# Kernel optimization log

Measured on AMD Instinct MI355X. Metric: run time of the kernel, lower is better.

## Reference

```python
import jax, jax.numpy as jnp
import numpy as np

B, H, V, L = 4096, 1024, 64, 16  # batch, hidden_size, msg_vocsize, max_msg_len


def setup_inputs() -> dict:
    key = jax.random.key(0)
    ks = jax.random.split(key, 10)
    s = 1.0 / np.sqrt(H)
    return {
        "encoder_hidden": jax.random.normal(ks[0], (B, H), jnp.float32),
        "encoder_cell": jax.random.normal(ks[1], (B, H), jnp.float32),
        "W_ih": jax.random.uniform(ks[2], (4 * H, H), jnp.float32, -s, s),
        "W_hh": jax.random.uniform(ks[3], (4 * H, H), jnp.float32, -s, s),
        "b_ih": jax.random.uniform(ks[4], (4 * H,), jnp.float32, -s, s),
        "b_hh": jax.random.uniform(ks[5], (4 * H,), jnp.float32, -s, s),
        "W_out": jax.random.uniform(ks[6], (V, H), jnp.float32, -s, s),
        "b_out": jax.random.uniform(ks[7], (V,), jnp.float32, -s, s),
        "init_input": jnp.zeros((1, H), jnp.float32),  # nn.Parameter initialized to zeros
        "msg_embedding": jax.random.normal(ks[8], (V, H), jnp.float32),
    }


def reference(encoder_hidden, encoder_cell, W_ih, W_hh, b_ih, b_hh,
              W_out, b_out, init_input, msg_embedding):
    batch = encoder_hidden.shape[0]
    x0 = jnp.broadcast_to(init_input, (batch, H))

    def step(carry, _):
        h, c, x, logp = carry
        x = jax.nn.relu(x)
        gates = x @ W_ih.T + b_ih + h @ W_hh.T + b_hh  # [B, 4H]
        i, f, g, o = jnp.split(gates, 4, axis=-1)      # torch LSTMCell gate order
        i, f, o = jax.nn.sigmoid(i), jax.nn.sigmoid(f), jax.nn.sigmoid(o)
        g = jnp.tanh(g)
        c = f * c + i * g
        h = o * jnp.tanh(c)
        logits = h @ W_out.T + b_out                   # [B, V]
        probs = jax.nn.softmax(logits, axis=1)
        pred = jax.nn.one_hot(jnp.argmax(probs, axis=1), V, dtype=probs.dtype)
        logp = logp + jnp.log(jnp.sum(probs * pred, axis=1))
        x = pred @ msg_embedding                       # [B, H]
        return (h, c, x, logp), (pred, logits)

    init = (encoder_hidden, encoder_cell, x0, jnp.zeros((batch,), encoder_hidden.dtype))
    (_, _, _, log_probs), (message, digits) = jax.lax.scan(step, init, None, length=L)
    mask = jnp.ones((L, 1, batch), encoder_hidden.dtype)
    return message, mask, digits, log_probs
```

## Files before the change

kernel.cpp:

```cpp
#include <hip/hip_runtime.h>
#include <math.h>

#define HD    1024
#define BATCH 4096
#define VOC   64
#define MSGL  16
#define KH    1024
#define NG    4096

typedef _Float16 f16;
typedef _Float16 f16x8 __attribute__((ext_vector_type(8)));
typedef _Float16 f16x4 __attribute__((ext_vector_type(4)));
typedef float    f32x4 __attribute__((ext_vector_type(4)));

__device__ __forceinline__ void splt(float v, f16& hi, f16& lo) {
    f16 h = (f16)v;
    hi = h;
    lo = (f16)(v - (float)h);
}

__device__ __forceinline__ float sigm_f(float x) {
    return __builtin_amdgcn_rcpf(1.0f + __builtin_amdgcn_exp2f(-1.44269504088896f * x));
}
__device__ __forceinline__ float tanh_f(float x) {
    return 1.0f - 2.0f * __builtin_amdgcn_rcpf(1.0f + __builtin_amdgcn_exp2f(2.88539008177793f * x));
}

__device__ __forceinline__ int orig_n(int np) {
    const int bxx = np >> 8, rem = np & 255;
    const int jh = rem >> 6, g = (rem >> 4) & 3, cnn = rem & 15;
    return g * 1024 + bxx * 64 + jh * 16 + cnn;
}
__device__ __forceinline__ int j_of(int np) {
    const int bxx = np >> 8, rem = np & 255;
    const int jh = rem >> 6, cnn = rem & 15;
    return bxx * 64 + jh * 16 + cnn;
}

__device__ __forceinline__ void async16(void* lds, const void* g) {
    __builtin_amdgcn_global_load_lds(
        (const __attribute__((address_space(1))) void*)g,
        (__attribute__((address_space(3))) void*)lds, 16, 0, 0);
}

__device__ __forceinline__ int swz(int row, int gran) {
    return row * 128 + ((gran ^ (row & 7)) << 4);
}

__device__ __forceinline__ void stage(char* ldsbase, const f16* hi, const f16* lo,
                                      int gbase, int k0, int r, int tid) {
    const int o   = (r * 512 + tid) * 16;
    const int row = o >> 7;
    const int gp  = (o >> 4) & 7;
    const int g   = gp ^ (row & 7);
    const f16* src = (g < 4 ? hi : lo) + (size_t)(gbase + row) * KH + k0 + (g & 3) * 8;
    async16(ldsbase + o, src);
}

__global__ __launch_bounds__(512, 2) void gemm_fused(
    const f16* __restrict__ Hh, const f16* __restrict__ Hl,
    const f16* __restrict__ Whi, const f16* __restrict__ Wlo,
    const float* __restrict__ XG, const int* __restrict__ ambuf,
    float* __restrict__ cbuf,
    f16* __restrict__ HhN, f16* __restrict__ HlN, int t)
{
    __shared__ char smem[132096];
    __shared__ int sAm[256];

    const int tid  = threadIdx.x;
    const int lane = tid & 63;
    const int wv   = tid >> 6;
    const int wm   = wv >> 2;
    const int wn   = wv & 3;
    const int bm   = blockIdx.y * 256;
    const int bnp  = blockIdx.x * 256;
    const int rl   = lane & 15;
    const int kg   = lane >> 4;

    f32x4 acc[8][4];
#pragma unroll
    for (int i = 0; i < 8; ++i)
#pragma unroll
        for (int g = 0; g < 4; ++g) acc[i][g] = f32x4{0.f, 0.f, 0.f, 0.f};

    if (tid < 256) sAm[tid] = (t == 0) ? 64 : ambuf[bm + tid];

#pragma unroll
    for (int r = 0; r < 4; ++r) stage(smem,         Hh,  Hl,  bm,  0, r, tid);
#pragma unroll
    for (int r = 0; r < 4; ++r) stage(smem + 32768, Whi, Wlo, bnp, 0, r, tid);

    for (int kt = 0; kt < 32; ++kt) {
        const char* cb = smem + (kt & 1) * 65536;
        char* nb = smem + ((kt + 1) & 1) * 65536;
        const int kn = ((kt + 1) & 31) * 32;

        asm volatile("s_waitcnt vmcnt(4)" ::: "memory");
        asm volatile("s_barrier" ::: "memory");

#pragma unroll
        for (int r = 0; r < 4; ++r) stage(nb, Hh, Hl, bm, kn, r, tid);

        asm volatile("s_waitcnt vmcnt(4)" ::: "memory");
        asm volatile("s_barrier" ::: "memory");

        f16x8 bh[4], bl[4];
#pragma unroll
        for (int f = 0; f < 4; ++f) {
            const int row = wn * 64 + f * 16 + rl;
            bh[f] = *(const f16x8*)(cb + 32768 + swz(row, kg));
            bl[f] = *(const f16x8*)(cb + 32768 + swz(row, kg + 4));
        }
#pragma unroll
        for (int r = 0; r < 4; ++r) stage(nb + 32768, Whi, Wlo, bnp, kn, r, tid);

        __builtin_amdgcn_s_setprio(1);
#pragma unroll
        for (int f = 0; f < 8; ++f) {
            const int row = wm * 128 + f * 16 + rl;
            const f16x8 ah = *(const f16x8*)(cb + swz(row, kg));
            const f16x8 al = *(const f16x8*)(cb + swz(row, kg + 4));
#pragma unroll
            for (int g = 0; g < 4; ++g) {
                acc[f][g] = __builtin_amdgcn_mfma_f32_16x16x32_f16(ah, bh[g], acc[f][g], 0, 0, 0);
                acc[f][g] = __builtin_amdgcn_mfma_f32_16x16x32_f16(ah, bl[g], acc[f][g], 0, 0, 0);
                acc[f][g] = __builtin_amdgcn_mfma_f32_16x16x32_f16(al, bh[g], acc[f][g], 0, 0, 0);
            }
        }
        __builtin_amdgcn_s_setprio(0);
    }

    asm volatile("s_waitcnt vmcnt(0)" ::: "memory");
    __syncthreads();

    float* sXG = (float*)smem;
    f16*   hHi = (f16*)(smem + 66560);
    f16*   hLo = (f16*)(smem + 99328);
    const int jb = blockIdx.x * 64;

#pragma unroll
    for (int i = 0; i < 9; ++i) {
        const int idx = i * 512 + tid;
        if (idx < 65 * 64) {
            const int v  = idx >> 6;
            const int c4 = (idx & 63) * 4;
            *(float4*)&sXG[v * 256 + c4] =
                *(const float4*)&XG[(size_t)v * NG + bnp + c4];
        }
    }
    __syncthreads();

    const int q    = lane >> 4;
    const int lcol = wn * 16 + rl;
    const int jglob = jb + lcol;
#pragma unroll
    for (int i = 0; i < 8; ++i) {
#pragma unroll
        for (int rg = 0; rg < 4; ++rg) {
            const int lrow = wm * 128 + i * 16 + q * 4 + rg;
            const int v = sAm[lrow];
            const float4 xg = *(const float4*)&sXG[v * 256 + lcol * 4];
            const size_t ci = (size_t)(bm + lrow) * HD + jglob;
            const float cold = cbuf[ci];
            const float I = sigm_f(acc[i][0][rg] + xg.x);
            const float F = sigm_f(acc[i][1][rg] + xg.y);
            const float G = tanh_f(acc[i][2][rg] + xg.z);
            const float O = sigm_f(acc[i][3][rg] + xg.w);
            const float cc = F * cold + I * G;
            const float hh = O * tanh_f(cc);
            cbuf[ci] = cc;
            f16 hi_, lo_;
            splt(hh, hi_, lo_);
            hHi[lrow * 64 + lcol] = hi_;
            hLo[lrow * 64 + lcol] = lo_;
        }
    }
    __syncthreads();

#pragma unroll
    for (int r = 0; r < 8; ++r) {
        const int idx = r * 512 + tid;
        const int row = idx >> 4;
        const int c4  = (idx & 15) * 4;
        *(f16x4*)&HhN[(size_t)(bm + row) * HD + jb + c4] = *(f16x4*)&hHi[row * 64 + c4];
        *(f16x4*)&HlN[(size_t)(bm + row) * HD + jb + c4] = *(f16x4*)&hLo[row * 64 + c4];
    }
}

__global__ __launch_bounds__(256) void logits_step(
    const f16* __restrict__ Hh, const f16* __restrict__ Hl,
    const float* __restrict__ W_outT, const float* __restrict__ b_out,
    float* __restrict__ omsg, float* __restrict__ odig,
    float* __restrict__ ologp, int* __restrict__ ambuf, int t)
{
    const int lane = threadIdx.x & 63;
    const int wv   = threadIdx.x >> 6;
    const int r0   = blockIdx.x * 8 + wv * 2;

    float a0 = 0.f, a1 = 0.f;
    const f16* hh0 = Hh + (size_t)r0 * HD;
    const f16* hl0 = Hl + (size_t)r0 * HD;
    const f16* hh1 = hh0 + HD;
    const f16* hl1 = hl0 + HD;
    for (int k = 0; k < HD; k += 4) {
        const float w0 = W_outT[(k + 0) * 64 + lane];
        const float w1 = W_outT[(k + 1) * 64 + lane];
        const float w2 = W_outT[(k + 2) * 64 + lane];
        const float w3 = W_outT[(k + 3) * 64 + lane];
        const f16x4 vh0 = *(const f16x4*)&hh0[k];
        const f16x4 vl0 = *(const f16x4*)&hl0[k];
        const f16x4 vh1 = *(const f16x4*)&hh1[k];
        const f16x4 vl1 = *(const f16x4*)&hl1[k];
        a0 += w0 * ((float)vh0[0] + (float)vl0[0]) + w1 * ((float)vh0[1] + (float)vl0[1])
            + w2 * ((float)vh0[2] + (float)vl0[2]) + w3 * ((float)vh0[3] + (float)vl0[3]);
        a1 += w0 * ((float)vh1[0] + (float)vl1[0]) + w1 * ((float)vh1[1] + (float)vl1[1])
            + w2 * ((float)vh1[2] + (float)vl1[2]) + w3 * ((float)vh1[3] + (float)vl1[3]);
    }
    const float bo = b_out[lane];
    const float accs[2] = {a0, a1};

#pragma unroll
    for (int r = 0; r < 2; ++r) {
        const int row = r0 + r;
        const float lg = accs[r] + bo;

        float m = lg; int am = lane;
#pragma unroll
        for (int d = 1; d < 64; d <<= 1) {
            const float om = __shfl_xor(m, d);
            const int   oa = __shfl_xor(am, d);
            if (om > m || (om == m && oa < am)) { m = om; am = oa; }
        }
        float s = expf(lg - m);
#pragma unroll
        for (int d = 1; d < 64; d <<= 1) s += __shfl_xor(s, d);

        odig[(size_t)row * VOC + lane] = lg;
        omsg[(size_t)row * VOC + lane] = (lane == am) ? 1.0f : 0.0f;
        if (lane == 0) {
            const float prev = (t == 0) ? 0.0f : ologp[row];
            ologp[row] = prev - logf(s);
            ambuf[row] = am;
        }
    }
}

__global__ __launch_bounds__(256) void xg_kernel(
    const float* __restrict__ W_ih, const float* __restrict__ rembT,
    const float* __restrict__ rembX0, const float* __restrict__ bR,
    float* __restrict__ XG)
{
    __shared__ float sW[4][1024];
    const int lane = threadIdx.x & 63;
    const int wv   = threadIdx.x >> 6;
    const int np   = blockIdx.x * 4 + wv;
    const int orig = orig_n(np);
    const float* wr = W_ih + (size_t)orig * HD;
#pragma unroll
    for (int c = 0; c < 4; ++c)
        *(float4*)&sW[wv][c * 256 + lane * 4] = *(const float4*)&wr[c * 256 + lane * 4];
    __syncthreads();

    float acc = 0.f, acc0 = 0.f;
#pragma unroll 4
    for (int k = 0; k < HD; ++k) {
        const float w = sW[wv][k];
        acc  += w * rembT[k * 64 + lane];
        acc0 += w * rembX0[k];
    }
    const float b = bR[np];
    const int g = (np >> 4) & 3;
    const int pos = j_of(np) * 4 + g;
    XG[(size_t)lane * NG + pos] = acc + b;
    if (lane == 0) XG[(size_t)64 * NG + pos] = acc0 + b;
}

__global__ __launch_bounds__(256) void prep_w(
    const float* __restrict__ W_hh, f16* __restrict__ Whi, f16* __restrict__ Wlo)
{
    const long long idx = ((long long)blockIdx.x * 256 + threadIdx.x) * 4;
    const int np = (int)(idx >> 10);
    const int k  = (int)(idx & 1023);
    const float4 v = *(const float4*)&W_hh[(size_t)orig_n(np) * HD + k];
    f16x4 vh, vl; f16 hi_, lo_;
    splt(v.x, hi_, lo_); vh[0] = hi_; vl[0] = lo_;
    splt(v.y, hi_, lo_); vh[1] = hi_; vl[1] = lo_;
    splt(v.z, hi_, lo_); vh[2] = hi_; vl[2] = lo_;
    splt(v.w, hi_, lo_); vh[3] = hi_; vl[3] = lo_;
    *(f16x4*)&Whi[idx] = vh;
    *(f16x4*)&Wlo[idx] = vl;
}

__global__ __launch_bounds__(256) void prep_h(
    const float* __restrict__ ench, f16* __restrict__ Hh, f16* __restrict__ Hl)
{
    const int idx = (blockIdx.x * 256 + threadIdx.x) * 4;
    const float4 v = *(const float4*)&ench[idx];
    f16x4 vh, vl; f16 hi_, lo_;
    splt(v.x, hi_, lo_); vh[0] = hi_; vl[0] = lo_;
    splt(v.y, hi_, lo_); vh[1] = hi_; vl[1] = lo_;
    splt(v.z, hi_, lo_); vh[2] = hi_; vl[2] = lo_;
    splt(v.w, hi_, lo_); vh[3] = hi_; vl[3] = lo_;
    *(f16x4*)&Hh[idx] = vh;
    *(f16x4*)&Hl[idx] = vl;
}

__global__ __launch_bounds__(256) void prep_c(
    const float* __restrict__ encc, float* __restrict__ cbuf)
{
    const int idx = (blockIdx.x * 256 + threadIdx.x) * 4;
    *(float4*)&cbuf[idx] = *(const float4*)&encc[idx];
}

__global__ __launch_bounds__(256) void prep_small(
    const float* __restrict__ W_out, const float* __restrict__ b_ih,
    const float* __restrict__ b_hh, const float* __restrict__ emb,
    const float* __restrict__ x0,
    float* __restrict__ W_outT, float* __restrict__ rembT,
    float* __restrict__ rembX0, float* __restrict__ bR, float* __restrict__ mask)
{
    const int i = blockIdx.x * 256 + threadIdx.x;
    mask[i] = 1.0f;
    const int v = i >> 10, k = i & 1023;
    W_outT[k * 64 + v] = W_out[i];
    rembT[k * 64 + v] = fmaxf(emb[i], 0.f);
    if (i < 1024) rembX0[i] = fmaxf(x0[i], 0.f);
    if (i < NG) {
        const int orig = orig_n(i);
        bR[i] = b_ih[orig] + b_hh[orig];
    }
}

extern "C" void kernel_launch(void* const* d_in, const int* in_sizes, int n_in,
                              void* d_out, int out_size, void* d_ws, size_t ws_size,
                              hipStream_t stream)
{
    const float* ench  = (const float*)d_in[0];
    const float* encc  = (const float*)d_in[1];
    const float* W_ih  = (const float*)d_in[2];
    const float* W_hh  = (const float*)d_in[3];
    const float* b_ih  = (const float*)d_in[4];
    const float* b_hh  = (const float*)d_in[5];
    const float* W_out = (const float*)d_in[6];
    const float* b_out = (const float*)d_in[7];
    const float* x0    = (const float*)d_in[8];
    const float* emb   = (const float*)d_in[9];
    float* out = (float*)d_out;

    char* ws = (char*)d_ws;
    f16*   Hh[2]  = { (f16*)(ws + ((size_t) 0 << 20)), (f16*)(ws + ((size_t)16 << 20)) };
    f16*   Hl[2]  = { (f16*)(ws + ((size_t) 8 << 20)), (f16*)(ws + ((size_t)24 << 20)) };
    f16*   Whr    = (f16*)(ws + ((size_t)32 << 20));
    f16*   Wlr    = (f16*)(ws + ((size_t)40 << 20));
    float* cbuf   = (float*)(ws + ((size_t)48 << 20));
    float* W_outT = (float*)(ws + ((size_t)64 << 20));
    float* rembT  = (float*)(ws + ((size_t)65 << 20));
    float* rembX0 = (float*)(ws + ((size_t)66 << 20));
    float* bR     = (float*)(ws + ((size_t)66 << 20) + 8192);
    float* XG     = (float*)(ws + ((size_t)67 << 20));
    int*   ambuf  = (int*)  (ws + ((size_t)69 << 20));

    float* out_msg0 = out;
    float* out_mask = out + (size_t)MSGL * BATCH * VOC;
    float* out_dig0 = out_mask + (size_t)MSGL * BATCH;
    float* out_logp = out_dig0 + (size_t)MSGL * BATCH * VOC;

    prep_w<<<4096, 256, 0, stream>>>(W_hh, Whr, Wlr);
    prep_h<<<4096, 256, 0, stream>>>(ench, Hh[0], Hl[0]);
    prep_c<<<4096, 256, 0, stream>>>(encc, cbuf);
    prep_small<<<256, 256, 0, stream>>>(W_out, b_ih, b_hh, emb, x0,
                                        W_outT, rembT, rembX0, bR, out_mask);
    xg_kernel<<<1024, 256, 0, stream>>>(W_ih, rembT, rembX0, bR, XG);

    for (int t = 0; t < MSGL; ++t) {
        const int cur = t & 1, nxt = cur ^ 1;
        gemm_fused<<<dim3(16, 16), 512, 0, stream>>>(
            Hh[cur], Hl[cur], Whr, Wlr, XG, ambuf, cbuf, Hh[nxt], Hl[nxt], t);
        logits_step<<<512, 256, 0, stream>>>(
            Hh[nxt], Hl[nxt], W_outT, b_out,
            out_msg0 + (size_t)t * BATCH * VOC,
            out_dig0 + (size_t)t * BATCH * VOC,
            out_logp, ambuf, t);
    }
}
```

Measured before the change: 2.359 ms.

## Switch gemm_fused to 128-row tiles with triple-buffered LDS pipeline

The recurrent GEMM tile is cut from 256x256 to 128x256 and the grid grows from 256 to 512 blocks launched as a 1D grid. The LDS pipeline goes from two buffers to three, prefetching two k-steps ahead with one barrier per iteration instead of two. This should give more blocks to fill the CUs and hide load latency better. In exchange, each block reuses the W tile over fewer rows, and LDS growing to 144KB drops occupancy to one block per CU.

```diff
diff --git a/kernel.cpp b/kernel.cpp
--- a/kernel.cpp
+++ b/kernel.cpp
@@ -48,8 +48,8 @@
 }
 
 __device__ __forceinline__ void stage(char* ldsbase, const f16* hi, const f16* lo,
-                                      int gbase, int k0, int r, int tid) {
-    const int o   = (r * 512 + tid) * 16;
+                                      int gbase, int k0, int idx) {
+    const int o   = idx * 16;
     const int row = o >> 7;
     const int gp  = (o >> 4) & 7;
     const int g   = gp ^ (row & 7);
@@ -57,69 +57,74 @@
     async16(ldsbase + o, src);
 }
 
-__global__ __launch_bounds__(512, 2) void gemm_fused(
+__global__ __launch_bounds__(512, 1) void gemm_fused(
     const f16* __restrict__ Hh, const f16* __restrict__ Hl,
     const f16* __restrict__ Whi, const f16* __restrict__ Wlo,
     const float* __restrict__ XG, const int* __restrict__ ambuf,
     float* __restrict__ cbuf,
     f16* __restrict__ HhN, f16* __restrict__ HlN, int t)
 {
-    __shared__ char smem[132096];
-    __shared__ int sAm[256];
+    __shared__ char smem[147456];
+    __shared__ int sAm[128];
 
     const int tid  = threadIdx.x;
     const int lane = tid & 63;
     const int wv   = tid >> 6;
     const int wm   = wv >> 2;
     const int wn   = wv & 3;
-    const int bm   = blockIdx.y * 256;
-    const int bnp  = blockIdx.x * 256;
+    const int d    = blockIdx.x;
+    const int by   = d >> 4;
+    const int bx   = d & 15;
+    const int bm   = by * 128;
+    const int bnp  = bx * 256;
     const int rl   = lane & 15;
     const int kg   = lane >> 4;
 
-    f32x4 acc[8][4];
-#pragma unroll
-    for (int i = 0; i < 8; ++i)
+    f32x4 acc[4][4];
+#pragma unroll
+    for (int i = 0; i < 4; ++i)
 #pragma unroll
         for (int g = 0; g < 4; ++g) acc[i][g] = f32x4{0.f, 0.f, 0.f, 0.f};
 
-    if (tid < 256) sAm[tid] = (t == 0) ? 64 : ambuf[bm + tid];
-
-#pragma unroll
-    for (int r = 0; r < 4; ++r) stage(smem,         Hh,  Hl,  bm,  0, r, tid);
-#pragma unroll
-    for (int r = 0; r < 4; ++r) stage(smem + 32768, Whi, Wlo, bnp, 0, r, tid);
+    if (tid < 128) sAm[tid] = (t == 0) ? 64 : ambuf[bm + tid];
+
+    char* s0 = smem;
+    char* s1 = smem + 49152;
+    char* s2 = smem + 98304;
+
+#pragma unroll
+    for (int r = 0; r < 2; ++r) stage(s0,         Hh,  Hl,  bm,  0,  r * 512 + tid);
+#pragma unroll
+    for (int r = 0; r < 4; ++r) stage(s0 + 16384, Whi, Wlo, bnp, 0,  r * 512 + tid);
+#pragma unroll
+    for (int r = 0; r < 2; ++r) stage(s1,         Hh,  Hl,  bm,  32, r * 512 + tid);
+#pragma unroll
+    for (int r = 0; r < 4; ++r) stage(s1 + 16384, Whi, Wlo, bnp, 32, r * 512 + tid);
 
     for (int kt = 0; kt < 32; ++kt) {
-        const char* cb = smem + (kt & 1) * 65536;
-        char* nb = smem + ((kt + 1) & 1) * 65536;
-        const int kn = ((kt + 1) & 31) * 32;
-
-        asm volatile("s_waitcnt vmcnt(4)" ::: "memory");
+        const int kn = ((kt + 2) & 31) * 32;
+
+        asm volatile("s_waitcnt vmcnt(6)" ::: "memory");
         asm volatile("s_barrier" ::: "memory");
 
 #pragma unroll
-        for (int r = 0; r < 4; ++r) stage(nb, Hh, Hl, bm, kn, r, tid);
-
-        asm volatile("s_waitcnt vmcnt(4)" ::: "memory");
-        asm volatile("s_barrier" ::: "memory");
+        for (int r = 0; r < 2; ++r) stage(s2,         Hh,  Hl,  bm,  kn, r * 512 + tid);
+#pragma unroll
+        for (int r = 0; r < 4; ++r) stage(s2 + 16384, Whi, Wlo, bnp, kn, r * 512 + tid);
 
         f16x8 bh[4], bl[4];
 #pragma unroll
+        for (int g = 0; g < 4; ++g) {
+            const int row = wn * 64 + g * 16 + rl;
+            bh[g] = *(const f16x8*)(s0 + 16384 + swz(row, kg));
+            bl[g] = *(const f16x8*)(s0 + 16384 + swz(row, kg + 4));
+        }
+        __builtin_amdgcn_s_setprio(1);
+#pragma unroll
         for (int f = 0; f < 4; ++f) {
-            const int row = wn * 64 + f * 16 + rl;
-            bh[f] = *(const f16x8*)(cb + 32768 + swz(row, kg));
-            bl[f] = *(const f16x8*)(cb + 32768 + swz(row, kg + 4));
-        }
-#pragma unroll
-        for (int r = 0; r < 4; ++r) stage(nb + 32768, Whi, Wlo, bnp, kn, r, tid);
-
-        __builtin_amdgcn_s_setprio(1);
-#pragma unroll
-        for (int f = 0; f < 8; ++f) {
-            const int row = wm * 128 + f * 16 + rl;
-            const f16x8 ah = *(const f16x8*)(cb + swz(row, kg));
-            const f16x8 al = *(const f16x8*)(cb + swz(row, kg + 4));
+            const int row = wm * 64 + f * 16 + rl;
+            const f16x8 ah = *(const f16x8*)(s0 + swz(row, kg));
+            const f16x8 al = *(const f16x8*)(s0 + swz(row, kg + 4));
 #pragma unroll
             for (int g = 0; g < 4; ++g) {
                 acc[f][g] = __builtin_amdgcn_mfma_f32_16x16x32_f16(ah, bh[g], acc[f][g], 0, 0, 0);
@@ -128,6 +133,8 @@
             }
         }
         __builtin_amdgcn_s_setprio(0);
+
+        char* tmp = s0; s0 = s1; s1 = s2; s2 = tmp;
     }
 
     asm volatile("s_waitcnt vmcnt(0)" ::: "memory");
@@ -135,8 +142,8 @@
 
     float* sXG = (float*)smem;
     f16*   hHi = (f16*)(smem + 66560);
-    f16*   hLo = (f16*)(smem + 99328);
-    const int jb = blockIdx.x * 64;
+    f16*   hLo = (f16*)(smem + 82944);
+    const int jb = bx * 64;
 
 #pragma unroll
     for (int i = 0; i < 9; ++i) {
@@ -154,10 +161,10 @@
     const int lcol = wn * 16 + rl;
     const int jglob = jb + lcol;
 #pragma unroll
-    for (int i = 0; i < 8; ++i) {
+    for (int i = 0; i < 4; ++i) {
 #pragma unroll
         for (int rg = 0; rg < 4; ++rg) {
-            const int lrow = wm * 128 + i * 16 + q * 4 + rg;
+            const int lrow = wm * 64 + i * 16 + q * 4 + rg;
             const int v = sAm[lrow];
             const float4 xg = *(const float4*)&sXG[v * 256 + lcol * 4];
             const size_t ci = (size_t)(bm + lrow) * HD + jglob;
@@ -178,7 +185,7 @@
     __syncthreads();
 
 #pragma unroll
-    for (int r = 0; r < 8; ++r) {
+    for (int r = 0; r < 4; ++r) {
         const int idx = r * 512 + tid;
         const int row = idx >> 4;
         const int c4  = (idx & 15) * 4;
@@ -374,7 +381,7 @@
 
     for (int t = 0; t < MSGL; ++t) {
         const int cur = t & 1, nxt = cur ^ 1;
-        gemm_fused<<<dim3(16, 16), 512, 0, stream>>>(
+        gemm_fused<<<512, 512, 0, stream>>>(
             Hh[cur], Hl[cur], Whr, Wlr, XG, ambuf, cbuf, Hh[nxt], Hl[nxt], t);
         logits_step<<<512, 256, 0, stream>>>(
             Hh[nxt], Hl[nxt], W_outT, b_out,
```

After: 2.663 ms. 1.13x slower.

## Fuse output-logits projection and argmax into the LSTM gate GEMM kernel

Applied to the files above, without the earlier changes.

Each gate-GEMM block now also accumulates the previous step's hidden state against a split-fp16 W_out tile, alongside the gate products. It then does the softmax, argmax and log-prob update in its epilogue and writes the outputs for step t-1. This removes the separate per-step logits kernel and the ambuf round-trip, keeping only one final logits launch for the last step. The cost is extra MFMA work, since every column block recomputes the same logits, plus more LDS and a launch_bounds change to one block per CU.

```diff
diff --git a/kernel.cpp b/kernel.cpp
--- a/kernel.cpp
+++ b/kernel.cpp
@@ -57,14 +57,17 @@
     async16(ldsbase + o, src);
 }
 
-__global__ __launch_bounds__(512, 2) void gemm_fused(
+__global__ __launch_bounds__(512, 1) void gemm_fused(
     const f16* __restrict__ Hh, const f16* __restrict__ Hl,
     const f16* __restrict__ Whi, const f16* __restrict__ Wlo,
-    const float* __restrict__ XG, const int* __restrict__ ambuf,
+    const f16* __restrict__ Wohi, const f16* __restrict__ Wolo,
+    const float* __restrict__ XG, const float* __restrict__ b_out,
     float* __restrict__ cbuf,
-    f16* __restrict__ HhN, f16* __restrict__ HlN, int t)
-{
-    __shared__ char smem[132096];
+    f16* __restrict__ HhN, f16* __restrict__ HlN,
+    float* __restrict__ omsg0, float* __restrict__ odig0,
+    float* __restrict__ ologp, int t)
+{
+    __shared__ char smem[147456];
     __shared__ int sAm[256];
 
     const int tid  = threadIdx.x;
@@ -72,27 +75,35 @@
     const int wv   = tid >> 6;
     const int wm   = wv >> 2;
     const int wn   = wv & 3;
-    const int bm   = blockIdx.y * 256;
-    const int bnp  = blockIdx.x * 256;
+    const int bx   = blockIdx.x;
+    const int by   = blockIdx.y;
+    const int bm   = by * 256;
+    const int bnp  = bx * 256;
     const int rl   = lane & 15;
     const int kg   = lane >> 4;
 
     f32x4 acc[8][4];
-#pragma unroll
-    for (int i = 0; i < 8; ++i)
+    f32x4 acc_l[8];
+#pragma unroll
+    for (int i = 0; i < 8; ++i) {
 #pragma unroll
         for (int g = 0; g < 4; ++g) acc[i][g] = f32x4{0.f, 0.f, 0.f, 0.f};
-
-    if (tid < 256) sAm[tid] = (t == 0) ? 64 : ambuf[bm + tid];
-
-#pragma unroll
-    for (int r = 0; r < 4; ++r) stage(smem,         Hh,  Hl,  bm,  0, r, tid);
-#pragma unroll
-    for (int r = 0; r < 4; ++r) stage(smem + 32768, Whi, Wlo, bnp, 0, r, tid);
+        acc_l[i] = f32x4{0.f, 0.f, 0.f, 0.f};
+    }
+
+#pragma unroll
+    for (int r = 0; r < 4; ++r) stage(smem,          Hh,   Hl,   bm,  0, r, tid);
+    stage(smem + 131072,                             Wohi, Wolo, 0,   0, 0, tid);
+#pragma unroll
+    for (int r = 0; r < 4; ++r) stage(smem + 65536,  Whi,  Wlo,  bnp, 0, r, tid);
 
     for (int kt = 0; kt < 32; ++kt) {
-        const char* cb = smem + (kt & 1) * 65536;
-        char* nb = smem + ((kt + 1) & 1) * 65536;
+        const char* cb  = smem + (kt & 1) * 32768;
+        const char* cbB = smem + 65536 + (kt & 1) * 32768;
+        const char* cbW = smem + 131072 + (kt & 1) * 8192;
+        char* nb  = smem + ((kt + 1) & 1) * 32768;
+        char* nbB = smem + 65536 + ((kt + 1) & 1) * 32768;
+        char* nbW = smem + 131072 + ((kt + 1) & 1) * 8192;
         const int kn = ((kt + 1) & 31) * 32;
 
         asm volatile("s_waitcnt vmcnt(4)" ::: "memory");
@@ -100,19 +111,22 @@
 
 #pragma unroll
         for (int r = 0; r < 4; ++r) stage(nb, Hh, Hl, bm, kn, r, tid);
-
-        asm volatile("s_waitcnt vmcnt(4)" ::: "memory");
+        stage(nbW, Wohi, Wolo, 0, kn, 0, tid);
+
+        asm volatile("s_waitcnt vmcnt(5)" ::: "memory");
         asm volatile("s_barrier" ::: "memory");
 
         f16x8 bh[4], bl[4];
 #pragma unroll
         for (int f = 0; f < 4; ++f) {
             const int row = wn * 64 + f * 16 + rl;
-            bh[f] = *(const f16x8*)(cb + 32768 + swz(row, kg));
-            bl[f] = *(const f16x8*)(cb + 32768 + swz(row, kg + 4));
-        }
-#pragma unroll
-        for (int r = 0; r < 4; ++r) stage(nb + 32768, Whi, Wlo, bnp, kn, r, tid);
+            bh[f] = *(const f16x8*)(cbB + swz(row, kg));
+            bl[f] = *(const f16x8*)(cbB + swz(row, kg + 4));
+        }
+        const f16x8 woh = *(const f16x8*)(cbW + swz(wn * 16 + rl, kg));
+        const f16x8 wol = *(const f16x8*)(cbW + swz(wn * 16 + rl, kg + 4));
+#pragma unroll
+        for (int r = 0; r < 4; ++r) stage(nbB, Whi, Wlo, bnp, kn, r, tid);
 
         __builtin_amdgcn_s_setprio(1);
 #pragma unroll
@@ -126,17 +140,71 @@
                 acc[f][g] = __builtin_amdgcn_mfma_f32_16x16x32_f16(ah, bl[g], acc[f][g], 0, 0, 0);
                 acc[f][g] = __builtin_amdgcn_mfma_f32_16x16x32_f16(al, bh[g], acc[f][g], 0, 0, 0);
             }
+            acc_l[f] = __builtin_amdgcn_mfma_f32_16x16x32_f16(ah, woh, acc_l[f], 0, 0, 0);
+            acc_l[f] = __builtin_amdgcn_mfma_f32_16x16x32_f16(ah, wol, acc_l[f], 0, 0, 0);
+            acc_l[f] = __builtin_amdgcn_mfma_f32_16x16x32_f16(al, woh, acc_l[f], 0, 0, 0);
         }
         __builtin_amdgcn_s_setprio(0);
     }
 
     asm volatile("s_waitcnt vmcnt(0)" ::: "memory");
     __syncthreads();
+
+    const int q = lane >> 4;
+
+    float* sL = (float*)smem;
+    if (t > 0) {
+        const int ti = t - 1;
+        const float bo = b_out[wn * 16 + rl];
+#pragma unroll
+        for (int f = 0; f < 8; ++f)
+#pragma unroll
+            for (int rg = 0; rg < 4; ++rg) {
+                const int row = wm * 128 + f * 16 + q * 4 + rg;
+                sL[row * 65 + wn * 16 + rl] = acc_l[f][rg] + bo;
+            }
+        __syncthreads();
+        if (tid < 256) {
+            const int row = tid;
+            float m = -1e30f; int am = 0;
+#pragma unroll 8
+            for (int c = 0; c < 64; ++c) {
+                const float v = sL[row * 65 + c];
+                if (v > m) { m = v; am = c; }
+            }
+            float s = 0.f;
+#pragma unroll 8
+            for (int c = 0; c < 64; ++c)
+                s += __builtin_amdgcn_exp2f(1.44269504088896f * (sL[row * 65 + c] - m));
+            sAm[row] = am;
+            if (bx == 0) {
+                const float prev = (ti == 0) ? 0.f : ologp[bm + row];
+                ologp[bm + row] = prev - logf(s);
+            }
+        }
+        __syncthreads();
+        if (bx == 0) {
+            float* omsg = omsg0 + (size_t)ti * BATCH * VOC;
+            float* odig = odig0 + (size_t)ti * BATCH * VOC;
+#pragma unroll
+            for (int i = 0; i < 8; ++i) {
+                const int idx = i * 512 + tid;
+                const int row = idx >> 6;
+                const int c   = idx & 63;
+                odig[(size_t)(bm + row) * VOC + c] = sL[row * 65 + c];
+                omsg[(size_t)(bm + row) * VOC + c] = (c == sAm[row]) ? 1.0f : 0.0f;
+            }
+        }
+        __syncthreads();
+    } else {
+        if (tid < 256) sAm[tid] = 64;
+        __syncthreads();
+    }
 
     float* sXG = (float*)smem;
     f16*   hHi = (f16*)(smem + 66560);
     f16*   hLo = (f16*)(smem + 99328);
-    const int jb = blockIdx.x * 64;
+    const int jb = bx * 64;
 
 #pragma unroll
     for (int i = 0; i < 9; ++i) {
@@ -150,7 +218,6 @@
     }
     __syncthreads();
 
-    const int q    = lane >> 4;
     const int lcol = wn * 16 + rl;
     const int jglob = jb + lcol;
 #pragma unroll
@@ -191,7 +258,7 @@
     const f16* __restrict__ Hh, const f16* __restrict__ Hl,
     const float* __restrict__ W_outT, const float* __restrict__ b_out,
     float* __restrict__ omsg, float* __restrict__ odig,
-    float* __restrict__ ologp, int* __restrict__ ambuf, int t)
+    float* __restrict__ ologp, int t)
 {
     const int lane = threadIdx.x & 63;
     const int wv   = threadIdx.x >> 6;
@@ -240,7 +307,6 @@
         if (lane == 0) {
             const float prev = (t == 0) ? 0.0f : ologp[row];
             ologp[row] = prev - logf(s);
-            ambuf[row] = am;
         }
     }
 }
@@ -316,13 +382,17 @@
     const float* __restrict__ W_out, const float* __restrict__ b_ih,
     const float* __restrict__ b_hh, const float* __restrict__ emb,
     const float* __restrict__ x0,
-    float* __restrict__ W_outT, float* __restrict__ rembT,
+    float* __restrict__ W_outT, f16* __restrict__ Wohi, f16* __restrict__ Wolo,
+    float* __restrict__ rembT,
     float* __restrict__ rembX0, float* __restrict__ bR, float* __restrict__ mask)
 {
     const int i = blockIdx.x * 256 + threadIdx.x;
     mask[i] = 1.0f;
     const int v = i >> 10, k = i & 1023;
-    W_outT[k * 64 + v] = W_out[i];
+    const float wo = W_out[i];
+    W_outT[k * 64 + v] = wo;
+    f16 hi2, lo2; splt(wo, hi2, lo2);
+    Wohi[i] = hi2; Wolo[i] = lo2;
     rembT[k * 64 + v] = fmaxf(emb[i], 0.f);
     if (i < 1024) rembX0[i] = fmaxf(x0[i], 0.f);
     if (i < NG) {
@@ -358,7 +428,8 @@
     float* rembX0 = (float*)(ws + ((size_t)66 << 20));
     float* bR     = (float*)(ws + ((size_t)66 << 20) + 8192);
     float* XG     = (float*)(ws + ((size_t)67 << 20));
-    int*   ambuf  = (int*)  (ws + ((size_t)69 << 20));
+    f16*   Wohi   = (f16*)(ws + ((size_t)70 << 20));
+    f16*   Wolo   = (f16*)(ws + ((size_t)71 << 20));
 
     float* out_msg0 = out;
     float* out_mask = out + (size_t)MSGL * BATCH * VOC;
@@ -369,17 +440,20 @@
     prep_h<<<4096, 256, 0, stream>>>(ench, Hh[0], Hl[0]);
     prep_c<<<4096, 256, 0, stream>>>(encc, cbuf);
     prep_small<<<256, 256, 0, stream>>>(W_out, b_ih, b_hh, emb, x0,
-                                        W_outT, rembT, rembX0, bR, out_mask);
+                                        W_outT, Wohi, Wolo, rembT, rembX0, bR,
+                                        out_mask);
     xg_kernel<<<1024, 256, 0, stream>>>(W_ih, rembT, rembX0, bR, XG);
 
     for (int t = 0; t < MSGL; ++t) {
         const int cur = t & 1, nxt = cur ^ 1;
         gemm_fused<<<dim3(16, 16), 512, 0, stream>>>(
-            Hh[cur], Hl[cur], Whr, Wlr, XG, ambuf, cbuf, Hh[nxt], Hl[nxt], t);
-        logits_step<<<512, 256, 0, stream>>>(
-            Hh[nxt], Hl[nxt], W_outT, b_out,
-            out_msg0 + (size_t)t * BATCH * VOC,
-            out_dig0 + (size_t)t * BATCH * VOC,
-            out_logp, ambuf, t);
-    }
-}
+            Hh[cur], Hl[cur], Whr, Wlr, Wohi, Wolo, XG, b_out,
+            cbuf, Hh[nxt], Hl[nxt],
+            out_msg0, out_dig0, out_logp, t);
+    }
+    logits_step<<<512, 256, 0, stream>>>(
+        Hh[0], Hl[0], W_outT, b_out,
+        out_msg0 + (size_t)(MSGL - 1) * BATCH * VOC,
+        out_dig0 + (size_t)(MSGL - 1) * BATCH * VOC,
+        out_logp, MSGL - 1);
+}
```

New measurement: 1.946 ms. -17.5%, faster.
